# Optimization experiments

Measured on AMD Instinct MI355X. Metric: run time of the kernel, lower is better.

The kernel has to match this reference:

```python
import jax, jax.numpy as jnp
import numpy as np

N_NODES = 50000
N_EDGES = 800000
D = 128
N_REL = 4
N_GRAPHS = 128
N_CLASSES = 16


def rgcn_layer(x, W_rel, W_root, b, src, dst, edge_type):
    # Per-relation transform of all nodes: [N, R, D]
    xt = jnp.einsum('nd,rdf->nrf', x, W_rel)
    msg = xt[src, edge_type]  # [E, D] gather message per edge
    # mean aggregation per (dst, relation) pair (PyG RGCNConv aggr='mean')
    seg = dst * N_REL + edge_type
    cnt = jax.ops.segment_sum(jnp.ones((src.shape[0],), x.dtype), seg,
                              num_segments=N_NODES * N_REL)
    norm = 1.0 / jnp.maximum(cnt[seg], 1.0)
    agg = jax.ops.segment_sum(msg * norm[:, None], dst, num_segments=N_NODES)
    return agg + x @ W_root + b


def setup_inputs() -> dict:
    key = jax.random.key(0)
    ks = jax.random.split(key, 12)
    s = 1.0 / np.sqrt(D)
    inp = {
        'x': jax.random.normal(ks[0], (N_NODES, D), jnp.float32),
        'edge_index': jax.random.randint(ks[1], (2, N_EDGES), 0, N_NODES, jnp.int64),
        'edge_type': jax.random.randint(ks[2], (N_EDGES,), 0, N_REL, jnp.int64),
        'batch': jnp.sort(jax.random.randint(ks[3], (N_NODES,), 0, N_GRAPHS, jnp.int64)),
        'W_rel1': jax.random.normal(ks[4], (N_REL, D, D), jnp.float32) * s,
        'W_root1': jax.random.normal(ks[5], (D, D), jnp.float32) * s,
        'b1': jnp.zeros((D,), jnp.float32),
        'W_rel2': jax.random.normal(ks[6], (N_REL, D, D), jnp.float32) * s,
        'W_root2': jax.random.normal(ks[7], (D, D), jnp.float32) * s,
        'b2': jnp.zeros((D,), jnp.float32),
        'W_cls': jax.random.normal(ks[8], (D, N_CLASSES), jnp.float32) * s,
        'b_cls': jnp.zeros((N_CLASSES,), jnp.float32),
    }
    return inp


def reference(x, edge_index, edge_type, batch, W_rel1, W_root1, b1,
              W_rel2, W_root2, b2, W_cls, b_cls):
    src, dst = edge_index[0], edge_index[1]
    h = jax.nn.relu(rgcn_layer(x, W_rel1, W_root1, b1, src, dst, edge_type))
    h = jax.nn.relu(rgcn_layer(h, W_rel2, W_root2, b2, src, dst, edge_type))
    # global mean pool over graphs (dropout is identity: training=False)
    gsum = jax.ops.segment_sum(h, batch, num_segments=N_GRAPHS)
    gcnt = jax.ops.segment_sum(jnp.ones((h.shape[0],), h.dtype), batch,
                               num_segments=N_GRAPHS)
    g = gsum / jnp.maximum(gcnt, 1.0)[:, None]
    return g @ W_cls + b_cls
```

## Files before the change

### kernel.cpp

```cpp
#include <hip/hip_runtime.h>

#define D_DIM 128
#define N_REL 4
#define CAP 32

typedef __attribute__((ext_vector_type(8))) short bf16x8;
typedef __attribute__((ext_vector_type(4))) float f32x4;

static inline int cdiv(int a, int b) { return (a + b - 1) / b; }

__device__ inline ushort f2bf(float f) {
    union { float f; unsigned u; } v;
    v.f = f;
    unsigned r = v.u + 0x7FFFu + ((v.u >> 16) & 1u);
    return (ushort)(r >> 16);
}

__device__ inline float bf2f(ushort u) {
    union { unsigned u; float f; } v;
    v.u = (unsigned)u << 16;
    return v.f;
}

__device__ inline float uif(unsigned u) {
    union { unsigned u; float f; } v;
    v.u = u;
    return v.f;
}

#define CNT_B 391
#define CAST_B 6250
#define PACK_B 80

__global__ __launch_bounds__(256) void prep_kernel(
    const float* __restrict__ x, ushort* __restrict__ Xb,
    const int* __restrict__ src, const int* __restrict__ dst,
    const int* __restrict__ et, unsigned* __restrict__ icnt,
    ushort* __restrict__ esorted,
    const float* __restrict__ Wrel1, const float* __restrict__ Wroot1,
    const float* __restrict__ Wrel2, const float* __restrict__ Wroot2,
    ushort* __restrict__ Wpk1, ushort* __restrict__ Wpk2,
    int n4, int nEdges) {
    int b = blockIdx.x;
    if (b < CNT_B) {
        int e = (b * 256 + threadIdx.x) * 8;
        if (e >= nEdges) return;
        if (e + 8 <= nEdges) {
            int4 sA = *(const int4*)(src + e);
            int4 sB = *(const int4*)(src + e + 4);
            int4 dA = *(const int4*)(dst + e);
            int4 dB = *(const int4*)(dst + e + 4);
            int4 tA = *(const int4*)(et + e);
            int4 tB = *(const int4*)(et + e + 4);
            unsigned o0 = atomicAdd(&icnt[dA.x], 1u << (8 * tA.x));
            unsigned o1 = atomicAdd(&icnt[dA.y], 1u << (8 * tA.y));
            unsigned o2 = atomicAdd(&icnt[dA.z], 1u << (8 * tA.z));
            unsigned o3 = atomicAdd(&icnt[dA.w], 1u << (8 * tA.w));
            unsigned o4 = atomicAdd(&icnt[dB.x], 1u << (8 * tB.x));
            unsigned o5 = atomicAdd(&icnt[dB.y], 1u << (8 * tB.y));
            unsigned o6 = atomicAdd(&icnt[dB.z], 1u << (8 * tB.z));
            unsigned o7 = atomicAdd(&icnt[dB.w], 1u << (8 * tB.w));
            int r0 = (int)(((o0 >> (8 * tA.x)) & 0xFFu) - 0xAAu);
            int r1 = (int)(((o1 >> (8 * tA.y)) & 0xFFu) - 0xAAu);
            int r2 = (int)(((o2 >> (8 * tA.z)) & 0xFFu) - 0xAAu);
            int r3 = (int)(((o3 >> (8 * tA.w)) & 0xFFu) - 0xAAu);
            int r4 = (int)(((o4 >> (8 * tB.x)) & 0xFFu) - 0xAAu);
            int r5 = (int)(((o5 >> (8 * tB.y)) & 0xFFu) - 0xAAu);
            int r6 = (int)(((o6 >> (8 * tB.z)) & 0xFFu) - 0xAAu);
            int r7 = (int)(((o7 >> (8 * tB.w)) & 0xFFu) - 0xAAu);
            esorted[((size_t)(dA.x * N_REL + tA.x) << 5) + r0] = (ushort)sA.x;
            esorted[((size_t)(dA.y * N_REL + tA.y) << 5) + r1] = (ushort)sA.y;
            esorted[((size_t)(dA.z * N_REL + tA.z) << 5) + r2] = (ushort)sA.z;
            esorted[((size_t)(dA.w * N_REL + tA.w) << 5) + r3] = (ushort)sA.w;
            esorted[((size_t)(dB.x * N_REL + tB.x) << 5) + r4] = (ushort)sB.x;
            esorted[((size_t)(dB.y * N_REL + tB.y) << 5) + r5] = (ushort)sB.y;
            esorted[((size_t)(dB.z * N_REL + tB.z) << 5) + r6] = (ushort)sB.z;
            esorted[((size_t)(dB.w * N_REL + tB.w) << 5) + r7] = (ushort)sB.w;
        } else {
            for (int j = 0; e + j < nEdges; ++j) {
                int dd = dst[e + j], tt = et[e + j];
                unsigned o = atomicAdd(&icnt[dd], 1u << (8 * tt));
                int r = (int)(((o >> (8 * tt)) & 0xFFu) - 0xAAu);
                esorted[((size_t)(dd * N_REL + tt) << 5) + r] = (ushort)src[e + j];
            }
        }
    } else if (b < CNT_B + CAST_B) {
        int i = (b - CNT_B) * 256 + threadIdx.x;
        if (i < n4) {
            float4 v = ((const float4*)x)[i];
            ushort4 o;
            o.x = f2bf(v.x); o.y = f2bf(v.y); o.z = f2bf(v.z); o.w = f2bf(v.w);
            ((ushort4*)Xb)[i] = o;
        }
    } else {
        int pb = b - (CNT_B + CAST_B);
        int layer = pb / 40;
        int rem = pb % 40;
        int mat = rem >> 3;
        int blk = rem & 7;
        const float* Wrel = layer ? Wrel2 : Wrel1;
        const float* Wroot = layer ? Wroot2 : Wroot1;
        ushort* out = layer ? Wpk2 : Wpk1;
        const float* W = (mat < N_REL) ? (Wrel + (size_t)mat * D_DIM * D_DIM) : Wroot;
        int t = blk * 256 + threadIdx.x;
        int lane = t & 63;
        int tile = t >> 6;
        int kt = tile >> 3;
        int nt = tile & 7;
        int n = nt * 16 + (lane & 15);
        int kb = kt * 32 + (lane >> 4) * 8;
        ushort* o = out + (((size_t)mat * 32 + tile) * 64 + lane) * 8;
        ushort4 lo, hi;
        lo.x = f2bf(W[(kb + 0) * D_DIM + n]);
        lo.y = f2bf(W[(kb + 1) * D_DIM + n]);
        lo.z = f2bf(W[(kb + 2) * D_DIM + n]);
        lo.w = f2bf(W[(kb + 3) * D_DIM + n]);
        hi.x = f2bf(W[(kb + 4) * D_DIM + n]);
        hi.y = f2bf(W[(kb + 5) * D_DIM + n]);
        hi.z = f2bf(W[(kb + 6) * D_DIM + n]);
        hi.w = f2bf(W[(kb + 7) * D_DIM + n]);
        *(ushort4*)(o) = lo;
        *(ushort4*)(o + 4) = hi;
    }
}

__global__ __launch_bounds__(256) void sort_kernel(
    const unsigned* __restrict__ icnt, ushort* __restrict__ esorted, int nseg) {
    __shared__ int ids[16][34];
    __shared__ int sids[16][34];
    const int tid = threadIdx.x;
    const int ql = tid & 15;
    const int qd = tid >> 4;
    const int seg = blockIdx.x * 16 + qd;
    if (seg >= nseg) return;
    unsigned w = icnt[seg >> 2];
    int deg = (int)(((w >> ((seg & 3) * 8)) & 0xFFu) - 0xAAu);
    if (deg < 2) return;
    ushort* row = esorted + ((size_t)seg << 5);
    unsigned u = ((const unsigned*)row)[ql];
    ids[qd][2 * ql] = (int)(u & 0xFFFFu);
    ids[qd][2 * ql + 1] = (int)(u >> 16);
    __threadfence_block();
#pragma unroll
    for (int base = 0; base < 2; ++base) {
        int j = base * 16 + ql;
        if (j < deg) {
            int v = ids[qd][j];
            int rank = 0;
            int k = 0;
            for (; k + 4 <= deg; k += 4) {
                int w0 = ids[qd][k], w1 = ids[qd][k + 1];
                int w2 = ids[qd][k + 2], w3 = ids[qd][k + 3];
                rank += (w0 < v || (w0 == v && k < j)) ? 1 : 0;
                rank += (w1 < v || (w1 == v && k + 1 < j)) ? 1 : 0;
                rank += (w2 < v || (w2 == v && k + 2 < j)) ? 1 : 0;
                rank += (w3 < v || (w3 == v && k + 3 < j)) ? 1 : 0;
            }
            for (; k < deg; ++k) {
                int wv = ids[qd][k];
                rank += (wv < v || (wv == v && k < j)) ? 1 : 0;
            }
            sids[qd][rank] = v;
        }
    }
    __threadfence_block();
    for (int j = ql; j < deg; j += 16) row[j] = (ushort)sids[qd][j];
}

__global__ __launch_bounds__(512) void layer_kernel(
    const ushort* __restrict__ Xb, const unsigned* __restrict__ icnt,
    const ushort* __restrict__ esorted, const ushort* __restrict__ Wpk,
    const float* __restrict__ bias, ushort* __restrict__ outb, int n_nodes) {
    __shared__ ushort Ms[32][520];
    __shared__ int ids[32][34];
    const int tid = threadIdx.x;
    const int wave = tid >> 6;
    const int lane = tid & 63;
    const int ql = tid & 15;
    const int qd = tid >> 4;
    const int m = lane & 15;
    const int q = lane >> 4;
    const int r0 = blockIdx.x * 32;
    const int rel = qd & 3;
    const int rbase = qd >> 2;

    unsigned id4[4], cnt4[4];
#pragma unroll
    for (int p = 0; p < 4; ++p) {
        int node = r0 + p * 8 + rbase;
        int vnode = min(node, n_nodes - 1);
        cnt4[p] = icnt[vnode];
        const ushort* eb = esorted + ((size_t)((vnode << 2) + rel) << 5);
        id4[p] = ((const unsigned*)eb)[ql];
        if (node >= n_nodes) cnt4[p] = 0xAAAAAAAAu;
    }

    auto acc8 = [](float* a, uint4 u) {
        a[0] += uif(u.x << 16); a[1] += uif(u.x & 0xFFFF0000u);
        a[2] += uif(u.y << 16); a[3] += uif(u.y & 0xFFFF0000u);
        a[4] += uif(u.z << 16); a[5] += uif(u.z & 0xFFFF0000u);
        a[6] += uif(u.w << 16); a[7] += uif(u.w & 0xFFFF0000u);
    };

    for (int p = 0; p < 4; ++p) {
        const int row = p * 8 + rbase;
        const int deg = (int)(((cnt4[p] >> (rel * 8)) & 0xFFu) - 0xAAu);
        uint4* mrow = (uint4*)&Ms[row][rel * 128 + ql * 8];
        const ushort* xb = Xb + ql * 8;
        if (deg <= 0) {
            *mrow = make_uint4(0u, 0u, 0u, 0u);
            continue;
        }
        ids[qd][2 * ql] = (int)(id4[p] & 0xFFFFu);
        ids[qd][2 * ql + 1] = (int)(id4[p] >> 16);
        __threadfence_block();
        float a[8], b[8];
#pragma unroll
        for (int j = 0; j < 8; ++j) { a[j] = 0.f; b[j] = 0.f; }
        int e = 0;
        for (; e + 8 <= deg; e += 8) {
            int s0 = ids[qd][e],     s1 = ids[qd][e + 1];
            int s2 = ids[qd][e + 2], s3 = ids[qd][e + 3];
            int s4 = ids[qd][e + 4], s5 = ids[qd][e + 5];
            int s6 = ids[qd][e + 6], s7 = ids[qd][e + 7];
            uint4 u0 = *(const uint4*)(xb + (size_t)s0 * D_DIM);
            uint4 u1 = *(const uint4*)(xb + (size_t)s1 * D_DIM);
            uint4 u2 = *(const uint4*)(xb + (size_t)s2 * D_DIM);
            uint4 u3 = *(const uint4*)(xb + (size_t)s3 * D_DIM);
            uint4 u4 = *(const uint4*)(xb + (size_t)s4 * D_DIM);
            uint4 u5 = *(const uint4*)(xb + (size_t)s5 * D_DIM);
            uint4 u6 = *(const uint4*)(xb + (size_t)s6 * D_DIM);
            uint4 u7 = *(const uint4*)(xb + (size_t)s7 * D_DIM);
            acc8(a, u0); acc8(b, u1); acc8(a, u2); acc8(b, u3);
            acc8(a, u4); acc8(b, u5); acc8(a, u6); acc8(b, u7);
        }
        if (e + 4 <= deg) {
            int s0 = ids[qd][e], s1 = ids[qd][e + 1];
            int s2 = ids[qd][e + 2], s3 = ids[qd][e + 3];
            uint4 u0 = *(const uint4*)(xb + (size_t)s0 * D_DIM);
            uint4 u1 = *(const uint4*)(xb + (size_t)s1 * D_DIM);
            uint4 u2 = *(const uint4*)(xb + (size_t)s2 * D_DIM);
            uint4 u3 = *(const uint4*)(xb + (size_t)s3 * D_DIM);
            acc8(a, u0); acc8(b, u1); acc8(a, u2); acc8(b, u3);
            e += 4;
        }
        if (e + 2 <= deg) {
            int s0 = ids[qd][e], s1 = ids[qd][e + 1];
            uint4 u0 = *(const uint4*)(xb + (size_t)s0 * D_DIM);
            uint4 u1 = *(const uint4*)(xb + (size_t)s1 * D_DIM);
            acc8(a, u0); acc8(b, u1);
            e += 2;
        }
        if (e < deg) {
            uint4 u0 = *(const uint4*)(xb + (size_t)ids[qd][e] * D_DIM);
            acc8(a, u0);
        }
        float sc = 1.0f / (float)deg;
        uint4 o;
        o.x = (unsigned)f2bf((a[0] + b[0]) * sc) | ((unsigned)f2bf((a[1] + b[1]) * sc) << 16);
        o.y = (unsigned)f2bf((a[2] + b[2]) * sc) | ((unsigned)f2bf((a[3] + b[3]) * sc) << 16);
        o.z = (unsigned)f2bf((a[4] + b[4]) * sc) | ((unsigned)f2bf((a[5] + b[5]) * sc) << 16);
        o.w = (unsigned)f2bf((a[6] + b[6]) * sc) | ((unsigned)f2bf((a[7] + b[7]) * sc) << 16);
        *mrow = o;
    }
    __syncthreads();

    f32x4 acc0 = (f32x4){0.f, 0.f, 0.f, 0.f};
    f32x4 acc1 = (f32x4){0.f, 0.f, 0.f, 0.f};
#pragma unroll
    for (int ph = 0; ph < N_REL; ++ph) {
#pragma unroll
        for (int kt = 0; kt < 4; ++kt) {
            bf16x8 b = *(const bf16x8*)(Wpk + (((size_t)ph * 32 + kt * 8 + wave) * 64 + lane) * 8);
            bf16x8 a0 = *(const bf16x8*)&Ms[m][ph * 128 + kt * 32 + q * 8];
            bf16x8 a1 = *(const bf16x8*)&Ms[16 + m][ph * 128 + kt * 32 + q * 8];
            acc0 = __builtin_amdgcn_mfma_f32_16x16x32_bf16(a0, b, acc0, 0, 0, 0);
            acc1 = __builtin_amdgcn_mfma_f32_16x16x32_bf16(a1, b, acc1, 0, 0, 0);
        }
    }
    {
        const int n0 = min(r0 + m, n_nodes - 1);
        const int n1 = min(r0 + 16 + m, n_nodes - 1);
        const ushort* aX0 = Xb + (size_t)n0 * D_DIM + q * 8;
        const ushort* aX1 = Xb + (size_t)n1 * D_DIM + q * 8;
#pragma unroll
        for (int kt = 0; kt < 4; ++kt) {
            bf16x8 b = *(const bf16x8*)(Wpk + (((size_t)N_REL * 32 + kt * 8 + wave) * 64 + lane) * 8);
            bf16x8 a0 = *(const bf16x8*)(aX0 + kt * 32);
            bf16x8 a1 = *(const bf16x8*)(aX1 + kt * 32);
            acc0 = __builtin_amdgcn_mfma_f32_16x16x32_bf16(a0, b, acc0, 0, 0, 0);
            acc1 = __builtin_amdgcn_mfma_f32_16x16x32_bf16(a1, b, acc1, 0, 0, 0);
        }
    }

    {
        int col = wave * 16 + m;
        float bv = bias[col];
#pragma unroll
        for (int rt = 0; rt < 2; ++rt) {
            const f32x4 av = rt ? acc1 : acc0;
#pragma unroll
            for (int r = 0; r < 4; ++r) {
                int row = r0 + rt * 16 + q * 4 + r;
                if (row < n_nodes)
                    outb[(size_t)row * D_DIM + col] = f2bf(fmaxf(av[r] + bv, 0.0f));
            }
        }
    }
}

__global__ __launch_bounds__(1024) void poolcls_kernel(
    const ushort* __restrict__ hb, const int* __restrict__ batch,
    const float* __restrict__ Wcls, const float* __restrict__ bcls,
    float* __restrict__ out, int n_nodes) {
    __shared__ float part[64][D_DIM + 1];
    __shared__ float mean[D_DIM];
    __shared__ float cpart[16][17];
    int g = blockIdx.x;
    int tid = threadIdx.x;
    int par = tid >> 4;
    int dg = (tid & 15) * 8;
    auto lb = [&](int val) {
        int lo = 0, hi = n_nodes;
        while (lo < hi) {
            int mid = (lo + hi) >> 1;
            if (batch[mid] < val) lo = mid + 1; else hi = mid;
        }
        return lo;
    };
    int lo = lb(g), hi = lb(g + 1);
    float a[8];
#pragma unroll
    for (int j = 0; j < 8; ++j) a[j] = 0.f;
    for (int nn = lo + par; nn < hi; nn += 64) {
        uint4 u = *(const uint4*)(hb + (size_t)nn * D_DIM + dg);
        a[0] += uif(u.x << 16); a[1] += uif(u.x & 0xFFFF0000u);
        a[2] += uif(u.y << 16); a[3] += uif(u.y & 0xFFFF0000u);
        a[4] += uif(u.z << 16); a[5] += uif(u.z & 0xFFFF0000u);
        a[6] += uif(u.w << 16); a[7] += uif(u.w & 0xFFFF0000u);
    }
#pragma unroll
    for (int j = 0; j < 8; ++j) part[par][dg + j] = a[j];
    __syncthreads();
    if (tid < D_DIM) {
        float s = 0.f;
#pragma unroll
        for (int j = 0; j < 64; ++j) s += part[j][tid];
        mean[tid] = s / fmaxf((float)(hi - lo), 1.0f);
    }
    __syncthreads();
    if (tid < 256) {
        int c = tid & 15, kc = tid >> 4;
        float s = 0.f;
#pragma unroll
        for (int j = 0; j < 8; ++j)
            s = fmaf(mean[kc * 8 + j], Wcls[(kc * 8 + j) * 16 + c], s);
        cpart[kc][c] = s;
    }
    __syncthreads();
    if (tid < 16) {
        float s = bcls[tid];
#pragma unroll
        for (int k = 0; k < 16; ++k) s += cpart[k][tid];
        out[g * 16 + tid] = s;
    }
}

extern "C" void kernel_launch(void* const* d_in, const int* in_sizes, int n_in,
                              void* d_out, int out_size, void* d_ws, size_t ws_size,
                              hipStream_t stream) {
    const float* x      = (const float*)d_in[0];
    const int*   ei     = (const int*)d_in[1];
    const int*   etype  = (const int*)d_in[2];
    const int*   batch  = (const int*)d_in[3];
    const float* Wrel1  = (const float*)d_in[4];
    const float* Wroot1 = (const float*)d_in[5];
    const float* b1     = (const float*)d_in[6];
    const float* Wrel2  = (const float*)d_in[7];
    const float* Wroot2 = (const float*)d_in[8];
    const float* b2     = (const float*)d_in[9];
    const float* Wcls   = (const float*)d_in[10];
    const float* bcls   = (const float*)d_in[11];
    float* out = (float*)d_out;

    const int N = in_sizes[0] / D_DIM;
    const int E = in_sizes[1] / 2;
    const int NSEG = N * N_REL;
    const int* src = ei;
    const int* dst = ei + E;

    ushort* Xb   = (ushort*)d_ws;
    ushort* h1b  = Xb + (size_t)N * D_DIM;
    ushort* h2b  = h1b + (size_t)N * D_DIM;
    ushort* Wpk1 = h2b + (size_t)N * D_DIM;
    ushort* Wpk2 = Wpk1 + 81920;
    unsigned* icnt = (unsigned*)(Wpk2 + 81920);
    ushort* esorted = (ushort*)(icnt + N);

    prep_kernel<<<CNT_B + CAST_B + PACK_B, 256, 0, stream>>>(
        x, Xb, src, dst, etype, icnt, esorted, Wrel1, Wroot1, Wrel2, Wroot2,
        Wpk1, Wpk2, N * D_DIM / 4, E);

    sort_kernel<<<cdiv(NSEG, 16), 256, 0, stream>>>(icnt, esorted, NSEG);

    layer_kernel<<<cdiv(N, 32), 512, 0, stream>>>(
        Xb, icnt, esorted, Wpk1, b1, h1b, N);

    layer_kernel<<<cdiv(N, 32), 512, 0, stream>>>(
        h1b, icnt, esorted, Wpk2, b2, h2b, N);

    poolcls_kernel<<<128, 1024, 0, stream>>>(h2b, batch, Wcls, bcls, out, N);
}
```

Before: 269.1 us.

## Restructure layer kernel to single-wave blocks gathering directly into MFMA fragments

```diff
diff --git a/kernel.cpp b/kernel.cpp
--- a/kernel.cpp
+++ b/kernel.cpp
@@ -167,33 +167,18 @@
     for (int j = ql; j < deg; j += 16) row[j] = (ushort)sids[qd][j];
 }
 
-__global__ __launch_bounds__(512) void layer_kernel(
+__global__ __launch_bounds__(64) void layer_kernel(
     const ushort* __restrict__ Xb, const unsigned* __restrict__ icnt,
     const ushort* __restrict__ esorted, const ushort* __restrict__ Wpk,
     const float* __restrict__ bias, ushort* __restrict__ outb, int n_nodes) {
-    __shared__ ushort Ms[32][520];
-    __shared__ int ids[32][34];
-    const int tid = threadIdx.x;
-    const int wave = tid >> 6;
-    const int lane = tid & 63;
-    const int ql = tid & 15;
-    const int qd = tid >> 4;
+    __shared__ ushort idsL[16][40];
+    const int lane = threadIdx.x;
     const int m = lane & 15;
     const int q = lane >> 4;
-    const int r0 = blockIdx.x * 32;
-    const int rel = qd & 3;
-    const int rbase = qd >> 2;
-
-    unsigned id4[4], cnt4[4];
-#pragma unroll
-    for (int p = 0; p < 4; ++p) {
-        int node = r0 + p * 8 + rbase;
-        int vnode = min(node, n_nodes - 1);
-        cnt4[p] = icnt[vnode];
-        const ushort* eb = esorted + ((size_t)((vnode << 2) + rel) << 5);
-        id4[p] = ((const unsigned*)eb)[ql];
-        if (node >= n_nodes) cnt4[p] = 0xAAAAAAAAu;
-    }
+    const int rbase = blockIdx.x * 16;
+    const int row = rbase + m;
+    const int node = min(row, n_nodes - 1);
+    const unsigned cw = icnt[node];
 
     auto acc8 = [](float* a, uint4 u) {
         a[0] += uif(u.x << 16); a[1] += uif(u.x & 0xFFFF0000u);
@@ -202,109 +187,85 @@
         a[6] += uif(u.w << 16); a[7] += uif(u.w & 0xFFFF0000u);
     };
 
-    for (int p = 0; p < 4; ++p) {
-        const int row = p * 8 + rbase;
-        const int deg = (int)(((cnt4[p] >> (rel * 8)) & 0xFFu) - 0xAAu);
-        uint4* mrow = (uint4*)&Ms[row][rel * 128 + ql * 8];
-        const ushort* xb = Xb + ql * 8;
-        if (deg <= 0) {
-            *mrow = make_uint4(0u, 0u, 0u, 0u);
-            continue;
-        }
-        ids[qd][2 * ql] = (int)(id4[p] & 0xFFFFu);
-        ids[qd][2 * ql + 1] = (int)(id4[p] >> 16);
+    f32x4 acc[8];
+#pragma unroll
+    for (int nt = 0; nt < 8; ++nt) acc[nt] = (f32x4){0.f, 0.f, 0.f, 0.f};
+
+    bf16x8 afrag[4];
+
+    for (int rel = 0; rel < N_REL; ++rel) {
+        const int deg = (int)(((cw >> (rel * 8)) & 0xFFu) - 0xAAu);
+        uint4 wst = *(const uint4*)(esorted + (((size_t)node * N_REL + rel) << 5) + q * 8);
+        *(uint4*)&idsL[m][q * 8] = wst;
         __threadfence_block();
-        float a[8], b[8];
-#pragma unroll
-        for (int j = 0; j < 8; ++j) { a[j] = 0.f; b[j] = 0.f; }
-        int e = 0;
-        for (; e + 8 <= deg; e += 8) {
-            int s0 = ids[qd][e],     s1 = ids[qd][e + 1];
-            int s2 = ids[qd][e + 2], s3 = ids[qd][e + 3];
-            int s4 = ids[qd][e + 4], s5 = ids[qd][e + 5];
-            int s6 = ids[qd][e + 6], s7 = ids[qd][e + 7];
-            uint4 u0 = *(const uint4*)(xb + (size_t)s0 * D_DIM);
-            uint4 u1 = *(const uint4*)(xb + (size_t)s1 * D_DIM);
-            uint4 u2 = *(const uint4*)(xb + (size_t)s2 * D_DIM);
-            uint4 u3 = *(const uint4*)(xb + (size_t)s3 * D_DIM);
-            uint4 u4 = *(const uint4*)(xb + (size_t)s4 * D_DIM);
-            uint4 u5 = *(const uint4*)(xb + (size_t)s5 * D_DIM);
-            uint4 u6 = *(const uint4*)(xb + (size_t)s6 * D_DIM);
-            uint4 u7 = *(const uint4*)(xb + (size_t)s7 * D_DIM);
-            acc8(a, u0); acc8(b, u1); acc8(a, u2); acc8(b, u3);
-            acc8(a, u4); acc8(b, u5); acc8(a, u6); acc8(b, u7);
-        }
-        if (e + 4 <= deg) {
-            int s0 = ids[qd][e], s1 = ids[qd][e + 1];
-            int s2 = ids[qd][e + 2], s3 = ids[qd][e + 3];
-            uint4 u0 = *(const uint4*)(xb + (size_t)s0 * D_DIM);
-            uint4 u1 = *(const uint4*)(xb + (size_t)s1 * D_DIM);
-            uint4 u2 = *(const uint4*)(xb + (size_t)s2 * D_DIM);
-            uint4 u3 = *(const uint4*)(xb + (size_t)s3 * D_DIM);
-            acc8(a, u0); acc8(b, u1); acc8(a, u2); acc8(b, u3);
-            e += 4;
-        }
-        if (e + 2 <= deg) {
-            int s0 = ids[qd][e], s1 = ids[qd][e + 1];
-            uint4 u0 = *(const uint4*)(xb + (size_t)s0 * D_DIM);
-            uint4 u1 = *(const uint4*)(xb + (size_t)s1 * D_DIM);
-            acc8(a, u0); acc8(b, u1);
-            e += 2;
-        }
-        if (e < deg) {
-            uint4 u0 = *(const uint4*)(xb + (size_t)ids[qd][e] * D_DIM);
-            acc8(a, u0);
-        }
-        float sc = 1.0f / (float)deg;
-        uint4 o;
-        o.x = (unsigned)f2bf((a[0] + b[0]) * sc) | ((unsigned)f2bf((a[1] + b[1]) * sc) << 16);
-        o.y = (unsigned)f2bf((a[2] + b[2]) * sc) | ((unsigned)f2bf((a[3] + b[3]) * sc) << 16);
-        o.z = (unsigned)f2bf((a[4] + b[4]) * sc) | ((unsigned)f2bf((a[5] + b[5]) * sc) << 16);
-        o.w = (unsigned)f2bf((a[6] + b[6]) * sc) | ((unsigned)f2bf((a[7] + b[7]) * sc) << 16);
-        *mrow = o;
-    }
-    __syncthreads();
-
-    f32x4 acc0 = (f32x4){0.f, 0.f, 0.f, 0.f};
-    f32x4 acc1 = (f32x4){0.f, 0.f, 0.f, 0.f};
-#pragma unroll
-    for (int ph = 0; ph < N_REL; ++ph) {
+        const float sc = deg > 0 ? 1.0f / (float)deg : 0.0f;
 #pragma unroll
         for (int kt = 0; kt < 4; ++kt) {
-            bf16x8 b = *(const bf16x8*)(Wpk + (((size_t)ph * 32 + kt * 8 + wave) * 64 + lane) * 8);
-            bf16x8 a0 = *(const bf16x8*)&Ms[m][ph * 128 + kt * 32 + q * 8];
-            bf16x8 a1 = *(const bf16x8*)&Ms[16 + m][ph * 128 + kt * 32 + q * 8];
-            acc0 = __builtin_amdgcn_mfma_f32_16x16x32_bf16(a0, b, acc0, 0, 0, 0);
-            acc1 = __builtin_amdgcn_mfma_f32_16x16x32_bf16(a1, b, acc1, 0, 0, 0);
-        }
-    }
-    {
-        const int n0 = min(r0 + m, n_nodes - 1);
-        const int n1 = min(r0 + 16 + m, n_nodes - 1);
-        const ushort* aX0 = Xb + (size_t)n0 * D_DIM + q * 8;
-        const ushort* aX1 = Xb + (size_t)n1 * D_DIM + q * 8;
+            const ushort* xb = Xb + kt * 32 + q * 8;
+            float a[8], b[8];
+#pragma unroll
+            for (int j = 0; j < 8; ++j) { a[j] = 0.f; b[j] = 0.f; }
+            int e = 0;
+            for (; e + 4 <= deg; e += 4) {
+                int s0 = idsL[m][e];
+                int s1 = idsL[m][e + 1];
+                int s2 = idsL[m][e + 2];
+                int s3 = idsL[m][e + 3];
+                uint4 u0 = *(const uint4*)(xb + (size_t)s0 * D_DIM);
+                uint4 u1 = *(const uint4*)(xb + (size_t)s1 * D_DIM);
+                uint4 u2 = *(const uint4*)(xb + (size_t)s2 * D_DIM);
+                uint4 u3 = *(const uint4*)(xb + (size_t)s3 * D_DIM);
+                acc8(a, u0); acc8(b, u1); acc8(a, u2); acc8(b, u3);
+            }
+            if (e + 2 <= deg) {
+                int s0 = idsL[m][e];
+                int s1 = idsL[m][e + 1];
+                uint4 u0 = *(const uint4*)(xb + (size_t)s0 * D_DIM);
+                uint4 u1 = *(const uint4*)(xb + (size_t)s1 * D_DIM);
+                acc8(a, u0); acc8(b, u1);
+                e += 2;
+            }
+            if (e < deg) {
+                uint4 u0 = *(const uint4*)(xb + (size_t)idsL[m][e] * D_DIM);
+                acc8(a, u0);
+            }
+            ushort p0 = f2bf((a[0] + b[0]) * sc), p1 = f2bf((a[1] + b[1]) * sc);
+            ushort p2 = f2bf((a[2] + b[2]) * sc), p3 = f2bf((a[3] + b[3]) * sc);
+            ushort p4 = f2bf((a[4] + b[4]) * sc), p5 = f2bf((a[5] + b[5]) * sc);
+            ushort p6 = f2bf((a[6] + b[6]) * sc), p7 = f2bf((a[7] + b[7]) * sc);
+            afrag[kt] = (bf16x8){(short)p0, (short)p1, (short)p2, (short)p3,
+                                 (short)p4, (short)p5, (short)p6, (short)p7};
+        }
+        __threadfence_block();
+#pragma unroll
+        for (int nt = 0; nt < 8; ++nt) {
+#pragma unroll
+            for (int kt = 0; kt < 4; ++kt) {
+                bf16x8 bf = *(const bf16x8*)(Wpk + (((size_t)rel * 32 + kt * 8 + nt) * 64 + lane) * 8);
+                acc[nt] = __builtin_amdgcn_mfma_f32_16x16x32_bf16(afrag[kt], bf, acc[nt], 0, 0, 0);
+            }
+        }
+    }
+#pragma unroll
+    for (int kt = 0; kt < 4; ++kt)
+        afrag[kt] = *(const bf16x8*)(Xb + (size_t)node * D_DIM + kt * 32 + q * 8);
+#pragma unroll
+    for (int nt = 0; nt < 8; ++nt) {
 #pragma unroll
         for (int kt = 0; kt < 4; ++kt) {
-            bf16x8 b = *(const bf16x8*)(Wpk + (((size_t)N_REL * 32 + kt * 8 + wave) * 64 + lane) * 8);
-            bf16x8 a0 = *(const bf16x8*)(aX0 + kt * 32);
-            bf16x8 a1 = *(const bf16x8*)(aX1 + kt * 32);
-            acc0 = __builtin_amdgcn_mfma_f32_16x16x32_bf16(a0, b, acc0, 0, 0, 0);
-            acc1 = __builtin_amdgcn_mfma_f32_16x16x32_bf16(a1, b, acc1, 0, 0, 0);
-        }
-    }
-
-    {
-        int col = wave * 16 + m;
+            bf16x8 bf = *(const bf16x8*)(Wpk + (((size_t)N_REL * 32 + kt * 8 + nt) * 64 + lane) * 8);
+            acc[nt] = __builtin_amdgcn_mfma_f32_16x16x32_bf16(afrag[kt], bf, acc[nt], 0, 0, 0);
+        }
+    }
+#pragma unroll
+    for (int nt = 0; nt < 8; ++nt) {
+        int col = nt * 16 + m;
         float bv = bias[col];
 #pragma unroll
-        for (int rt = 0; rt < 2; ++rt) {
-            const f32x4 av = rt ? acc1 : acc0;
-#pragma unroll
-            for (int r = 0; r < 4; ++r) {
-                int row = r0 + rt * 16 + q * 4 + r;
-                if (row < n_nodes)
-                    outb[(size_t)row * D_DIM + col] = f2bf(fmaxf(av[r] + bv, 0.0f));
-            }
+        for (int r = 0; r < 4; ++r) {
+            int orow = rbase + q * 4 + r;
+            if (orow < n_nodes)
+                outb[(size_t)orow * D_DIM + col] = f2bf(fmaxf(acc[nt][r] + bv, 0.0f));
         }
     }
 }
@@ -403,10 +364,10 @@
 
     sort_kernel<<<cdiv(NSEG, 16), 256, 0, stream>>>(icnt, esorted, NSEG);
 
-    layer_kernel<<<cdiv(N, 32), 512, 0, stream>>>(
+    layer_kernel<<<cdiv(N, 16), 64, 0, stream>>>(
         Xb, icnt, esorted, Wpk1, b1, h1b, N);
 
-    layer_kernel<<<cdiv(N, 32), 512, 0, stream>>>(
+    layer_kernel<<<cdiv(N, 16), 64, 0, stream>>>(
         h1b, icnt, esorted, Wpk2, b2, h2b, N);
 
     poolcls_kernel<<<128, 1024, 0, stream>>>(h2b, batch, Wcls, bcls, out, N);
```

New measurement: 336.2 us. 24.9% more time.

## Shrink layer blocks to 16 rows with 256 threads and preload packed edge ids

Applied to the files above, without the earlier changes.

```diff
diff --git a/kernel.cpp b/kernel.cpp
--- a/kernel.cpp
+++ b/kernel.cpp
@@ -167,12 +167,12 @@
     for (int j = ql; j < deg; j += 16) row[j] = (ushort)sids[qd][j];
 }
 
-__global__ __launch_bounds__(512) void layer_kernel(
+__global__ __launch_bounds__(256, 6) void layer_kernel(
     const ushort* __restrict__ Xb, const unsigned* __restrict__ icnt,
     const ushort* __restrict__ esorted, const ushort* __restrict__ Wpk,
     const float* __restrict__ bias, ushort* __restrict__ outb, int n_nodes) {
-    __shared__ ushort Ms[32][520];
-    __shared__ int ids[32][34];
+    __shared__ ushort Ms[16][520];
+    __shared__ unsigned idsU[16][4][17];
     const int tid = threadIdx.x;
     const int wave = tid >> 6;
     const int lane = tid & 63;
@@ -180,20 +180,21 @@
     const int qd = tid >> 4;
     const int m = lane & 15;
     const int q = lane >> 4;
-    const int r0 = blockIdx.x * 32;
+    const int r0 = blockIdx.x * 16;
     const int rel = qd & 3;
-    const int rbase = qd >> 2;
-
-    unsigned id4[4], cnt4[4];
+    const int rowgrp = qd >> 2;
+
+    unsigned cw4[4];
 #pragma unroll
     for (int p = 0; p < 4; ++p) {
-        int node = r0 + p * 8 + rbase;
+        int node = r0 + p * 4 + rowgrp;
         int vnode = min(node, n_nodes - 1);
-        cnt4[p] = icnt[vnode];
-        const ushort* eb = esorted + ((size_t)((vnode << 2) + rel) << 5);
-        id4[p] = ((const unsigned*)eb)[ql];
-        if (node >= n_nodes) cnt4[p] = 0xAAAAAAAAu;
-    }
+        cw4[p] = (node < n_nodes) ? icnt[vnode] : 0xAAAAAAAAu;
+        unsigned idw = ((const unsigned*)(esorted +
+                        (((size_t)vnode * N_REL + rel) << 5)))[ql];
+        idsU[qd][p][ql] = idw;
+    }
+    __threadfence_block();
 
     auto acc8 = [](float* a, uint4 u) {
         a[0] += uif(u.x << 16); a[1] += uif(u.x & 0xFFFF0000u);
@@ -202,57 +203,46 @@
         a[6] += uif(u.w << 16); a[7] += uif(u.w & 0xFFFF0000u);
     };
 
+    const ushort* xb = Xb + ql * 8;
+#pragma unroll
     for (int p = 0; p < 4; ++p) {
-        const int row = p * 8 + rbase;
-        const int deg = (int)(((cnt4[p] >> (rel * 8)) & 0xFFu) - 0xAAu);
+        const int row = p * 4 + rowgrp;
+        const int deg = (int)(((cw4[p] >> (rel * 8)) & 0xFFu) - 0xAAu);
         uint4* mrow = (uint4*)&Ms[row][rel * 128 + ql * 8];
-        const ushort* xb = Xb + ql * 8;
         if (deg <= 0) {
             *mrow = make_uint4(0u, 0u, 0u, 0u);
             continue;
         }
-        ids[qd][2 * ql] = (int)(id4[p] & 0xFFFFu);
-        ids[qd][2 * ql + 1] = (int)(id4[p] >> 16);
-        __threadfence_block();
+        const unsigned* idp = idsU[qd][p];
         float a[8], b[8];
 #pragma unroll
         for (int j = 0; j < 8; ++j) { a[j] = 0.f; b[j] = 0.f; }
         int e = 0;
-        for (; e + 8 <= deg; e += 8) {
-            int s0 = ids[qd][e],     s1 = ids[qd][e + 1];
-            int s2 = ids[qd][e + 2], s3 = ids[qd][e + 3];
-            int s4 = ids[qd][e + 4], s5 = ids[qd][e + 5];
-            int s6 = ids[qd][e + 6], s7 = ids[qd][e + 7];
-            uint4 u0 = *(const uint4*)(xb + (size_t)s0 * D_DIM);
-            uint4 u1 = *(const uint4*)(xb + (size_t)s1 * D_DIM);
-            uint4 u2 = *(const uint4*)(xb + (size_t)s2 * D_DIM);
-            uint4 u3 = *(const uint4*)(xb + (size_t)s3 * D_DIM);
-            uint4 u4 = *(const uint4*)(xb + (size_t)s4 * D_DIM);
-            uint4 u5 = *(const uint4*)(xb + (size_t)s5 * D_DIM);
-            uint4 u6 = *(const uint4*)(xb + (size_t)s6 * D_DIM);
-            uint4 u7 = *(const uint4*)(xb + (size_t)s7 * D_DIM);
+        for (; e + 4 <= deg; e += 4) {
+            unsigned w0 = idp[e >> 1];
+            unsigned w1 = idp[(e >> 1) + 1];
+            size_t s0 = (size_t)(w0 & 0xFFFFu) * D_DIM;
+            size_t s1 = (size_t)(w0 >> 16) * D_DIM;
+            size_t s2 = (size_t)(w1 & 0xFFFFu) * D_DIM;
+            size_t s3 = (size_t)(w1 >> 16) * D_DIM;
+            uint4 u0 = *(const uint4*)(xb + s0);
+            uint4 u1 = *(const uint4*)(xb + s1);
+            uint4 u2 = *(const uint4*)(xb + s2);
+            uint4 u3 = *(const uint4*)(xb + s3);
             acc8(a, u0); acc8(b, u1); acc8(a, u2); acc8(b, u3);
-            acc8(a, u4); acc8(b, u5); acc8(a, u6); acc8(b, u7);
-        }
-        if (e + 4 <= deg) {
-            int s0 = ids[qd][e], s1 = ids[qd][e + 1];
-            int s2 = ids[qd][e + 2], s3 = ids[qd][e + 3];
-            uint4 u0 = *(const uint4*)(xb + (size_t)s0 * D_DIM);
-            uint4 u1 = *(const uint4*)(xb + (size_t)s1 * D_DIM);
-            uint4 u2 = *(const uint4*)(xb + (size_t)s2 * D_DIM);
-            uint4 u3 = *(const uint4*)(xb + (size_t)s3 * D_DIM);
-            acc8(a, u0); acc8(b, u1); acc8(a, u2); acc8(b, u3);
-            e += 4;
         }
         if (e + 2 <= deg) {
-            int s0 = ids[qd][e], s1 = ids[qd][e + 1];
-            uint4 u0 = *(const uint4*)(xb + (size_t)s0 * D_DIM);
-            uint4 u1 = *(const uint4*)(xb + (size_t)s1 * D_DIM);
+            unsigned w0 = idp[e >> 1];
+            size_t s0 = (size_t)(w0 & 0xFFFFu) * D_DIM;
+            size_t s1 = (size_t)(w0 >> 16) * D_DIM;
+            uint4 u0 = *(const uint4*)(xb + s0);
+            uint4 u1 = *(const uint4*)(xb + s1);
             acc8(a, u0); acc8(b, u1);
             e += 2;
         }
         if (e < deg) {
-            uint4 u0 = *(const uint4*)(xb + (size_t)ids[qd][e] * D_DIM);
+            size_t s0 = (size_t)(idp[e >> 1] & 0xFFFFu) * D_DIM;
+            uint4 u0 = *(const uint4*)(xb + s0);
             acc8(a, u0);
         }
         float sc = 1.0f / (float)deg;
@@ -271,40 +261,36 @@
     for (int ph = 0; ph < N_REL; ++ph) {
 #pragma unroll
         for (int kt = 0; kt < 4; ++kt) {
-            bf16x8 b = *(const bf16x8*)(Wpk + (((size_t)ph * 32 + kt * 8 + wave) * 64 + lane) * 8);
-            bf16x8 a0 = *(const bf16x8*)&Ms[m][ph * 128 + kt * 32 + q * 8];
-            bf16x8 a1 = *(const bf16x8*)&Ms[16 + m][ph * 128 + kt * 32 + q * 8];
-            acc0 = __builtin_amdgcn_mfma_f32_16x16x32_bf16(a0, b, acc0, 0, 0, 0);
-            acc1 = __builtin_amdgcn_mfma_f32_16x16x32_bf16(a1, b, acc1, 0, 0, 0);
+            bf16x8 a = *(const bf16x8*)&Ms[m][ph * 128 + kt * 32 + q * 8];
+            bf16x8 b0 = *(const bf16x8*)(Wpk + (((size_t)ph * 32 + kt * 8 + wave * 2) * 64 + lane) * 8);
+            bf16x8 b1 = *(const bf16x8*)(Wpk + (((size_t)ph * 32 + kt * 8 + wave * 2 + 1) * 64 + lane) * 8);
+            acc0 = __builtin_amdgcn_mfma_f32_16x16x32_bf16(a, b0, acc0, 0, 0, 0);
+            acc1 = __builtin_amdgcn_mfma_f32_16x16x32_bf16(a, b1, acc1, 0, 0, 0);
         }
     }
     {
         const int n0 = min(r0 + m, n_nodes - 1);
-        const int n1 = min(r0 + 16 + m, n_nodes - 1);
-        const ushort* aX0 = Xb + (size_t)n0 * D_DIM + q * 8;
-        const ushort* aX1 = Xb + (size_t)n1 * D_DIM + q * 8;
+        const ushort* aX = Xb + (size_t)n0 * D_DIM + q * 8;
 #pragma unroll
         for (int kt = 0; kt < 4; ++kt) {
-            bf16x8 b = *(const bf16x8*)(Wpk + (((size_t)N_REL * 32 + kt * 8 + wave) * 64 + lane) * 8);
-            bf16x8 a0 = *(const bf16x8*)(aX0 + kt * 32);
-            bf16x8 a1 = *(const bf16x8*)(aX1 + kt * 32);
-            acc0 = __builtin_amdgcn_mfma_f32_16x16x32_bf16(a0, b, acc0, 0, 0, 0);
-            acc1 = __builtin_amdgcn_mfma_f32_16x16x32_bf16(a1, b, acc1, 0, 0, 0);
-        }
-    }
-
-    {
-        int col = wave * 16 + m;
+            bf16x8 a = *(const bf16x8*)(aX + kt * 32);
+            bf16x8 b0 = *(const bf16x8*)(Wpk + (((size_t)N_REL * 32 + kt * 8 + wave * 2) * 64 + lane) * 8);
+            bf16x8 b1 = *(const bf16x8*)(Wpk + (((size_t)N_REL * 32 + kt * 8 + wave * 2 + 1) * 64 + lane) * 8);
+            acc0 = __builtin_amdgcn_mfma_f32_16x16x32_bf16(a, b0, acc0, 0, 0, 0);
+            acc1 = __builtin_amdgcn_mfma_f32_16x16x32_bf16(a, b1, acc1, 0, 0, 0);
+        }
+    }
+
+#pragma unroll
+    for (int j = 0; j < 2; ++j) {
+        const f32x4 av = j ? acc1 : acc0;
+        int col = (wave * 2 + j) * 16 + m;
         float bv = bias[col];
 #pragma unroll
-        for (int rt = 0; rt < 2; ++rt) {
-            const f32x4 av = rt ? acc1 : acc0;
-#pragma unroll
-            for (int r = 0; r < 4; ++r) {
-                int row = r0 + rt * 16 + q * 4 + r;
-                if (row < n_nodes)
-                    outb[(size_t)row * D_DIM + col] = f2bf(fmaxf(av[r] + bv, 0.0f));
-            }
+        for (int r = 0; r < 4; ++r) {
+            int orow = r0 + q * 4 + r;
+            if (orow < n_nodes)
+                outb[(size_t)orow * D_DIM + col] = f2bf(fmaxf(av[r] + bv, 0.0f));
         }
     }
 }
@@ -403,10 +389,10 @@
 
     sort_kernel<<<cdiv(NSEG, 16), 256, 0, stream>>>(icnt, esorted, NSEG);
 
-    layer_kernel<<<cdiv(N, 32), 512, 0, stream>>>(
+    layer_kernel<<<cdiv(N, 16), 256, 0, stream>>>(
         Xb, icnt, esorted, Wpk1, b1, h1b, N);
 
-    layer_kernel<<<cdiv(N, 32), 512, 0, stream>>>(
+    layer_kernel<<<cdiv(N, 16), 256, 0, stream>>>(
         h1b, icnt, esorted, Wpk2, b2, h2b, N);
 
     poolcls_kernel<<<128, 1024, 0, stream>>>(h2b, batch, Wcls, bcls, out, N);
```

Result: faster. 251.6 us (-6.5%).
